# Performance work log

Hardware: AMD Instinct MI355X
Metric: run time of the kernel (lower is better)

## Reference

```python
import jax, jax.numpy as jnp
import numpy as np

N = 100000   # nodes
R = 4        # relation types
E = 200000   # edges per relation
IN, HID, OUT = 128, 256, 256


def _hetero_conv(x, ew, src, dst, W, b):
    """One HeteroGraphConv(mean) layer of GraphConv(norm='both') per relation.
    x: [N, d_in], ew: [R, E, d_in], src/dst: [R, E], W: [R, d_in, d_out], b: [R, d_out]."""
    outs = []
    for r in range(R):  # small fixed relation set
        s, d = src[r], dst[r]
        ones = jnp.ones((E,), x.dtype)
        deg_out = jax.ops.segment_sum(ones, s, num_segments=N)
        deg_in = jax.ops.segment_sum(ones, d, num_segments=N)
        ns = jax.lax.rsqrt(jnp.clip(deg_out, 1.0))  # src-side norm
        nd = jax.lax.rsqrt(jnp.clip(deg_in, 1.0))   # dst-side norm
        # gather src feats, scale, edge-weight, scatter-sum to dst
        m = x[s] * ns[s][:, None] * ew[r]                       # [E, d_in]
        agg = jax.ops.segment_sum(m, d, num_segments=N)          # [N, d_in]
        agg = agg * nd[:, None]
        outs.append(agg @ W[r] + b[r])
    return sum(outs) / R


def setup_inputs() -> dict:
    key = jax.random.key(0)
    ks = jax.random.split(key, 12)
    sc = 0.05
    return {
        "node_feat": jax.random.normal(ks[0], (N, IN), jnp.float32),
        "edge_w_raw": jax.random.normal(ks[1], (R, E, IN), jnp.float32),
        "src": jax.random.randint(ks[2], (R, E), 0, N),
        "dst": jax.random.randint(ks[3], (R, E), 0, N),
        "Wn": jax.random.normal(ks[4], (IN, HID), jnp.float32) * sc,
        "bn": jax.random.normal(ks[5], (HID,), jnp.float32) * sc,
        "Wr": jax.random.normal(ks[6], (IN, HID), jnp.float32) * sc,
        "br": jax.random.normal(ks[7], (HID,), jnp.float32) * sc,
        "W1": jax.random.normal(ks[8], (R, HID, HID), jnp.float32) * sc,
        "b1": jax.random.normal(ks[9], (R, HID), jnp.float32) * sc,
        "W2": jax.random.normal(ks[10], (R, HID, OUT), jnp.float32) * sc,
        "b2": jax.random.normal(ks[11], (R, OUT), jnp.float32) * sc,
    }


def reference(node_feat, edge_w_raw, src, dst, Wn, bn, Wr, br, W1, b1, W2, b2):
    # rela_fc on raw edge weights (shared by both layers)
    ew = jnp.einsum('rei,ih->reh', edge_w_raw, Wr) + br          # [R, E, HID]
    # node_fc
    x0 = node_feat @ Wn + bn                                      # [N, HID]
    h1 = _hetero_conv(x0, ew, src, dst, W1, b1)                   # [N, HID]
    h2 = _hetero_conv(h1, ew, src, dst, W2, b2)                   # [N, OUT]
    return h2
```

## Files before the change

### kernel.cpp

```cpp
#include <hip/hip_runtime.h>

constexpr int Nn  = 100000;
constexpr int Rr  = 4;
constexpr int Ee  = 200000;
constexpr int Din = 128;
constexpr int Dh  = 256;
constexpr int RN  = Rr * Nn;
constexpr int RE  = Rr * Ee;

typedef float  f32x4  __attribute__((ext_vector_type(4)));
typedef __bf16 bf16x4 __attribute__((ext_vector_type(4)));
typedef __bf16 bf16x8 __attribute__((ext_vector_type(8)));

__global__ __launch_bounds__(256) void count_deg_kernel(
    const int* __restrict__ src, const int* __restrict__ dst,
    int* __restrict__ dego, int* __restrict__ degi) {
  int i = blockIdx.x * 256 + threadIdx.x;
  if (i < RE) {
    int r = i / Ee;
    atomicAdd(&dego[r * Nn + src[i]], 1);
    atomicAdd(&degi[r * Nn + dst[i]], 1);
  }
}

__global__ __launch_bounds__(256) void norms_kernel(
    const int* __restrict__ dego, const int* __restrict__ degi,
    float* __restrict__ ns, float* __restrict__ nd) {
  int i = blockIdx.x * 256 + threadIdx.x;
  if (i < RN) {
    int a = dego[i]; if (a < 1) a = 1;
    int b = degi[i]; if (b < 1) b = 1;
    ns[i] = rsqrtf((float)a);
    nd[i] = rsqrtf((float)b);
  }
}

__device__ inline int block_excl_scan_256(int tsum, int tid, int* wsum) {
  int lane = tid & 63, w = tid >> 6;
  int inc = tsum;
#pragma unroll
  for (int off = 1; off < 64; off <<= 1) {
    int t = __shfl_up(inc, off);
    if (lane >= off) inc += t;
  }
  if (lane == 63) wsum[w] = inc;
  __syncthreads();
  int woff = 0;
  for (int i = 0; i < w; ++i) woff += wsum[i];
  return woff + inc - tsum;
}

__global__ __launch_bounds__(256) void scan1_kernel(
    const int* __restrict__ in, int* __restrict__ out,
    int* __restrict__ partials, int n) {
  __shared__ int wsum[4];
  int tid = threadIdx.x;
  int base = blockIdx.x * 1024 + tid * 4;
  int v[4];
#pragma unroll
  for (int j = 0; j < 4; ++j) v[j] = (base + j < n) ? in[base + j] : 0;
  int tsum = v[0] + v[1] + v[2] + v[3];
  int off = block_excl_scan_256(tsum, tid, wsum);
  int run = off;
#pragma unroll
  for (int j = 0; j < 4; ++j) {
    if (base + j < n) out[base + j] = run;
    run += v[j];
  }
  __syncthreads();
  if (tid == 0) partials[blockIdx.x] = wsum[0] + wsum[1] + wsum[2] + wsum[3];
}

__global__ __launch_bounds__(256) void scan2_kernel(int* __restrict__ p, int n) {
  __shared__ int wsum[4];
  int tid = threadIdx.x;
  int e0 = (2 * tid     < n) ? p[2 * tid]     : 0;
  int e1 = (2 * tid + 1 < n) ? p[2 * tid + 1] : 0;
  int off = block_excl_scan_256(e0 + e1, tid, wsum);
  if (2 * tid     < n) p[2 * tid]     = off;
  if (2 * tid + 1 < n) p[2 * tid + 1] = off + e0;
}

__global__ __launch_bounds__(256) void scan3_kernel(
    int* __restrict__ out, const int* __restrict__ partials, int n) {
  int i = blockIdx.x * 256 + threadIdx.x;
  if (i < n) out[i] += partials[i >> 10];
  if (i == 0) out[n] = RE;
}

__global__ __launch_bounds__(256) void fill_eid_kernel(
    const int* __restrict__ dst, int* __restrict__ cursor,
    int* __restrict__ eid) {
  int i = blockIdx.x * 256 + threadIdx.x;
  if (i < RE) {
    int r = i / Ee;
    int pos = atomicAdd(&cursor[r * Nn + dst[i]], 1);
    eid[pos] = i;
  }
}

__global__ __launch_bounds__(256) void bias_combine_kernel(
    const float* __restrict__ b1, const float* __restrict__ b2,
    float* __restrict__ cb) {
  int i = threadIdx.x;
  cb[i]      = 0.25f * (b1[i] + b1[Dh + i] + b1[2 * Dh + i] + b1[3 * Dh + i]);
  cb[Dh + i] = 0.25f * (b2[i] + b2[Dh + i] + b2[2 * Dh + i] + b2[3 * Dh + i]);
}

__global__ __launch_bounds__(256) void transpose_bf16_kernel(
    const float* __restrict__ in, __bf16* __restrict__ outp, int K) {
  __shared__ float t[32][33];
  int kb = blockIdx.x * 32, nb = blockIdx.y * 32;
  int tx = threadIdx.x & 31, ty = threadIdx.x >> 5;
#pragma unroll
  for (int j = 0; j < 32; j += 8)
    t[ty + j][tx] = in[(size_t)(kb + ty + j) * Dh + nb + tx];
  __syncthreads();
#pragma unroll
  for (int j = 0; j < 32; j += 8)
    outp[(size_t)(nb + ty + j) * K + kb + tx] = (__bf16)t[tx][ty + j];
}

template <int K, bool ABF16, bool OUT_BF16>
__global__ __launch_bounds__(256) void gemm_stream(
    const void* __restrict__ Av, const __bf16* __restrict__ Bt,
    void* __restrict__ Cv, const float* __restrict__ bias,
    float alpha, int M) {
  const int tid  = threadIdx.x;
  const int w    = tid >> 6;
  const int lane = tid & 63;
  const int l15  = lane & 15, quad = lane >> 4;
  const int m0   = blockIdx.x * 64;
  const int n0   = w * 64;

  f32x4 acc[4][4] = {};

  int arow[4];
#pragma unroll
  for (int mt = 0; mt < 4; ++mt) {
    int r = m0 + mt * 16 + l15;
    arow[mt] = (r < M) ? r : (M - 1);
  }

#pragma unroll 4
  for (int kt = 0; kt < K / 32; ++kt) {
    const int kk = kt * 32 + quad * 8;
    bf16x8 bfrag[4];
#pragma unroll
    for (int nt = 0; nt < 4; ++nt) {
      int n = n0 + nt * 16 + l15;
      bfrag[nt] = *(const bf16x8*)(Bt + (size_t)n * K + kk);
    }
    bf16x8 afrag[4];
    if constexpr (ABF16) {
      const __bf16* A = (const __bf16*)Av;
#pragma unroll
      for (int mt = 0; mt < 4; ++mt)
        afrag[mt] = *(const bf16x8*)(A + (size_t)arow[mt] * K + kk);
    } else {
      const float* A = (const float*)Av;
#pragma unroll
      for (int mt = 0; mt < 4; ++mt) {
        const float* ap = A + (size_t)arow[mt] * K + kk;
        f32x4 v0 = *(const f32x4*)(ap);
        f32x4 v1 = *(const f32x4*)(ap + 4);
        bf16x8 t;
        t[0] = (__bf16)v0[0]; t[1] = (__bf16)v0[1];
        t[2] = (__bf16)v0[2]; t[3] = (__bf16)v0[3];
        t[4] = (__bf16)v1[0]; t[5] = (__bf16)v1[1];
        t[6] = (__bf16)v1[2]; t[7] = (__bf16)v1[3];
        afrag[mt] = t;
      }
    }
#pragma unroll
    for (int mt = 0; mt < 4; ++mt)
#pragma unroll
      for (int nt = 0; nt < 4; ++nt)
        acc[mt][nt] = __builtin_amdgcn_mfma_f32_16x16x32_bf16(
            afrag[mt], bfrag[nt], acc[mt][nt], 0, 0, 0);
  }

#pragma unroll
  for (int mt = 0; mt < 4; ++mt) {
    int rl = m0 + mt * 16 + quad * 4;
#pragma unroll
    for (int nt = 0; nt < 4; ++nt) {
      int col = n0 + nt * 16 + l15;
      float bv = bias ? bias[col] : 0.f;
#pragma unroll
      for (int ri = 0; ri < 4; ++ri) {
        int grow = rl + ri;
        if (grow < M) {
          size_t idx = (size_t)grow * Dh + col;
          float v = alpha * acc[mt][nt][ri] + bv;
          if constexpr (OUT_BF16) {
            ((__bf16*)Cv)[idx] = (__bf16)v;
          } else {
            ((float*)Cv)[idx] = v;
          }
        }
      }
    }
  }
}

__global__ __launch_bounds__(256) void aggregate4_kernel(
    const float* __restrict__ x, const __bf16* __restrict__ ew,
    const int* __restrict__ src, const int* __restrict__ rowptr,
    const int* __restrict__ eid, const float* __restrict__ ns,
    const float* __restrict__ nd, __bf16* __restrict__ agg4) {
  int g = blockIdx.x * 4 + (threadIdx.x >> 6);
  if (g >= RN) return;
  int r = g / Nn;
  int n = g - r * Nn;
  int lane = threadIdx.x & 63;
  int p0 = rowptr[g], p1 = rowptr[g + 1];
  const float* nsr = ns + (size_t)r * Nn;
  f32x4 acc = {0.f, 0.f, 0.f, 0.f};
  for (int p = p0; p < p1; p += 2) {
    int  geA  = eid[p];
    bool hasB = (p + 1 < p1);
    int  geB  = hasB ? eid[p + 1] : geA;
    int sA = src[geA];
    int sB = src[geB];
    float scA = nsr[sA];
    float scB = hasB ? nsr[sB] : 0.f;
    f32x4  xA = *(const f32x4*)(x + (size_t)sA * Dh + lane * 4);
    bf16x4 eA = *(const bf16x4*)(ew + (size_t)geA * Dh + lane * 4);
    f32x4  xB = *(const f32x4*)(x + (size_t)sB * Dh + lane * 4);
    bf16x4 eB = *(const bf16x4*)(ew + (size_t)geB * Dh + lane * 4);
    acc[0] += xA[0] * scA * (float)eA[0] + xB[0] * scB * (float)eB[0];
    acc[1] += xA[1] * scA * (float)eA[1] + xB[1] * scB * (float)eB[1];
    acc[2] += xA[2] * scA * (float)eA[2] + xB[2] * scB * (float)eB[2];
    acc[3] += xA[3] * scA * (float)eA[3] + xB[3] * scB * (float)eB[3];
  }
  float ndv = nd[g];
  bf16x4 o;
  o[0] = (__bf16)(acc[0] * ndv);
  o[1] = (__bf16)(acc[1] * ndv);
  o[2] = (__bf16)(acc[2] * ndv);
  o[3] = (__bf16)(acc[3] * ndv);
  *(bf16x4*)(agg4 + (size_t)n * (4 * Dh) + (size_t)r * Dh + lane * 4) = o;
}

__global__ __launch_bounds__(256) void edge_scatter_kernel(
    const float* __restrict__ x, const __bf16* __restrict__ ew,
    const int* __restrict__ src, const int* __restrict__ dst,
    const float* __restrict__ ns, const float* __restrict__ nd,
    float* __restrict__ aggf, int cnt) {
  int e = blockIdx.x * 4 + (threadIdx.x >> 6);
  if (e >= cnt) return;
  int lane = threadIdx.x & 63;
  int s = src[e], d = dst[e];
  float sc = ns[s] * nd[d];
  f32x4 xv = *(const f32x4*)(x + (size_t)s * Dh + lane * 4);
  bf16x4 ev = *(const bf16x4*)(ew + (size_t)e * Dh + lane * 4);
  float* ap = aggf + (size_t)d * Dh + lane * 4;
  atomicAdd(ap + 0, xv[0] * sc * (float)ev[0]);
  atomicAdd(ap + 1, xv[1] * sc * (float)ev[1]);
  atomicAdd(ap + 2, xv[2] * sc * (float)ev[2]);
  atomicAdd(ap + 3, xv[3] * sc * (float)ev[3]);
}

__global__ __launch_bounds__(256) void pack_agg_kernel(
    const float* __restrict__ aggf, __bf16* __restrict__ agg4, int r) {
  int i = blockIdx.x * 256 + threadIdx.x;
  if (i < Nn * 64) {
    int n = i >> 6;
    int c = (i & 63) * 4;
    f32x4 v = *(const f32x4*)(aggf + (size_t)n * Dh + c);
    bf16x4 o;
    o[0] = (__bf16)v[0]; o[1] = (__bf16)v[1];
    o[2] = (__bf16)v[2]; o[3] = (__bf16)v[3];
    *(bf16x4*)(agg4 + (size_t)n * (4 * Dh) + (size_t)r * Dh + c) = o;
  }
}

extern "C" void kernel_launch(void* const* d_in, const int* in_sizes, int n_in,
                              void* d_out, int out_size, void* d_ws, size_t ws_size,
                              hipStream_t stream) {
  const float* node_feat  = (const float*)d_in[0];
  const float* edge_w_raw = (const float*)d_in[1];
  const int*   src        = (const int*)d_in[2];
  const int*   dst        = (const int*)d_in[3];
  const float* Wn = (const float*)d_in[4];
  const float* bn = (const float*)d_in[5];
  const float* Wr = (const float*)d_in[6];
  const float* br = (const float*)d_in[7];
  const float* W1 = (const float*)d_in[8];
  const float* b1 = (const float*)d_in[9];
  const float* W2 = (const float*)d_in[10];
  const float* b2 = (const float*)d_in[11];
  float* out = (float*)d_out;

  char* ws = (char*)d_ws;
  size_t off = 0;
  auto alloc = [&](size_t bytes) -> void* {
    void* p = ws + off;
    off += (bytes + 255) & ~(size_t)255;
    return p;
  };
  float*  ns     = (float*)alloc(sizeof(float) * RN);
  float*  nd     = (float*)alloc(sizeof(float) * RN);
  int*    rowptr = (int*)alloc(sizeof(int) * (RN + 1));
  int*    cursor = (int*)alloc(sizeof(int) * RN);
  int*    eid    = (int*)alloc(sizeof(int) * RE);
  int*    parts  = (int*)alloc(sizeof(int) * 512);
  float*  cb     = (float*)alloc(sizeof(float) * 2 * Dh);
  __bf16* BtWn   = (__bf16*)alloc(sizeof(__bf16) * (size_t)Din * Dh);
  __bf16* BtWr   = (__bf16*)alloc(sizeof(__bf16) * (size_t)Din * Dh);
  __bf16* BtW1   = (__bf16*)alloc(sizeof(__bf16) * (size_t)(4 * Dh) * Dh);
  __bf16* BtW2   = (__bf16*)alloc(sizeof(__bf16) * (size_t)(4 * Dh) * Dh);
  float*  x0     = (float*)alloc(sizeof(float) * (size_t)Nn * Dh);
  float*  h1     = (float*)alloc(sizeof(float) * (size_t)Nn * Dh);
  __bf16* agg4   = (__bf16*)alloc(sizeof(__bf16) * (size_t)Nn * 4 * Dh);
  size_t fixed = off;
  size_t ew_full_bytes = (size_t)RE * Dh * 2;
  bool full = (fixed + ew_full_bytes) <= ws_size;
  __bf16* ewb  = nullptr;
  float*  aggf = nullptr;
  int CH = Ee;
  if (full) {
    ewb = (__bf16*)alloc(ew_full_bytes);
  } else {
    aggf = (float*)alloc(sizeof(float) * (size_t)Nn * Dh);
    size_t avail = ws_size > off ? ws_size - off : 0;
    size_t ch = avail / ((size_t)Dh * 2);
    ch = (ch / 512) * 512;
    if (ch > (size_t)Ee) ch = (size_t)Ee;
    if (ch < 512) ch = 512;
    CH = (int)ch;
    ewb = (__bf16*)alloc((size_t)CH * Dh * 2);
  }

  int* dego = (int*)agg4;
  int* degi = dego + RN;
  hipMemsetAsync(dego, 0, sizeof(int) * 2 * (size_t)RN, stream);
  count_deg_kernel<<<(RE + 255) / 256, 256, 0, stream>>>(src, dst, dego, degi);
  norms_kernel<<<(RN + 255) / 256, 256, 0, stream>>>(dego, degi, ns, nd);

  int nchunks = (RN + 1023) / 1024;
  scan1_kernel<<<nchunks, 256, 0, stream>>>(degi, rowptr, parts, RN);
  scan2_kernel<<<1, 256, 0, stream>>>(parts, nchunks);
  scan3_kernel<<<(RN + 255) / 256, 256, 0, stream>>>(rowptr, parts, RN);
  hipMemcpyAsync(cursor, rowptr, sizeof(int) * RN, hipMemcpyDeviceToDevice, stream);
  fill_eid_kernel<<<(RE + 255) / 256, 256, 0, stream>>>(dst, cursor, eid);

  bias_combine_kernel<<<1, 256, 0, stream>>>(b1, b2, cb);
  transpose_bf16_kernel<<<dim3(Din / 32, Dh / 32), 256, 0, stream>>>(Wn, BtWn, Din);
  transpose_bf16_kernel<<<dim3(Din / 32, Dh / 32), 256, 0, stream>>>(Wr, BtWr, Din);
  transpose_bf16_kernel<<<dim3(4 * Dh / 32, Dh / 32), 256, 0, stream>>>(W1, BtW1, 4 * Dh);
  transpose_bf16_kernel<<<dim3(4 * Dh / 32, Dh / 32), 256, 0, stream>>>(W2, BtW2, 4 * Dh);

  gemm_stream<Din, false, false><<<(Nn + 63) / 64, 256, 0, stream>>>(
      node_feat, BtWn, x0, bn, 1.0f, Nn);

  if (full) {
    gemm_stream<Din, false, true><<<RE / 64, 256, 0, stream>>>(
        edge_w_raw, BtWr, ewb, br, 1.0f, RE);
  }

  for (int layer = 0; layer < 2; ++layer) {
    const float*  x   = layer ? h1 : x0;
    float*        o   = layer ? out : h1;
    const __bf16* Bt  = layer ? BtW2 : BtW1;
    const float*  cbl = cb + layer * Dh;
    if (full) {
      aggregate4_kernel<<<(RN + 3) / 4, 256, 0, stream>>>(
          x, ewb, src, rowptr, eid, ns, nd, agg4);
    } else {
      for (int r = 0; r < Rr; ++r) {
        hipMemsetAsync(aggf, 0, sizeof(float) * (size_t)Nn * Dh, stream);
        for (int c0 = 0; c0 < Ee; c0 += CH) {
          int cnt = (Ee - c0 < CH) ? (Ee - c0) : CH;
          gemm_stream<Din, false, true><<<(cnt + 63) / 64, 256, 0, stream>>>(
              edge_w_raw + ((size_t)r * Ee + c0) * Din, BtWr, ewb, br, 1.0f, cnt);
          edge_scatter_kernel<<<(cnt + 3) / 4, 256, 0, stream>>>(
              x, ewb, src + (size_t)r * Ee + c0, dst + (size_t)r * Ee + c0,
              ns + (size_t)r * Nn, nd + (size_t)r * Nn, aggf, cnt);
        }
        pack_agg_kernel<<<(Nn * 64 + 255) / 256, 256, 0, stream>>>(aggf, agg4, r);
      }
    }
    gemm_stream<4 * Dh, true, false><<<(Nn + 63) / 64, 256, 0, stream>>>(
        agg4, Bt, o, cbl, 0.25f, Nn);
  }
}
```

Before: 2.146 ms.

## Rewrite GEMMs with double-buffered LDS staging and persistent tiles

Replaces the direct-from-global GEMM with a kernel that stages A tiles into swizzled LDS using global_load_lds and double-buffers them, so loads for the next tile or K-slice overlap the MFMA work on the current one. The f32-input GEMMs become persistent: a 512-block grid loops over M tiles and keeps the B fragments in registers across tiles. The bf16 K=1024 GEMM pipelines over K chunks. The cost is more LDS per block (up to 64KB), hand-placed waitcnt and barriers, and a risk of lower occupancy.

```diff
diff --git a/kernel.cpp b/kernel.cpp
--- a/kernel.cpp
+++ b/kernel.cpp
@@ -121,86 +121,172 @@
     outp[(size_t)(nb + ty + j) * K + kb + tx] = (__bf16)t[tx][ty + j];
 }
 
+typedef __attribute__((address_space(1))) const void* gas_p;
+typedef __attribute__((address_space(3))) void* las_p;
+
+__device__ inline void gload_lds16(const void* g, void* l) {
+  __builtin_amdgcn_global_load_lds((gas_p)g, (las_p)l, 16, 0, 0);
+}
+
+__device__ inline void barrier_sync() {
+  asm volatile("" ::: "memory");
+  __builtin_amdgcn_s_barrier();
+  __builtin_amdgcn_sched_barrier(0);
+  asm volatile("" ::: "memory");
+}
+
 template <int K, bool ABF16, bool OUT_BF16>
-__global__ __launch_bounds__(256) void gemm_stream(
+__global__ __launch_bounds__(256, 2) void gemm_pipe(
     const void* __restrict__ Av, const __bf16* __restrict__ Bt,
     void* __restrict__ Cv, const float* __restrict__ bias,
-    float alpha, int M) {
+    float alpha, int M, int mtiles) {
+  constexpr int BUFB = ABF16 ? 16384 : 32768;
+  constexpr int ROWB = ABF16 ? 256 : 512;
+  constexpr int EB   = ABF16 ? 2 : 4;
+  constexpr int G    = BUFB / (256 * 16);
+  __shared__ __align__(16) char smem[2][BUFB];
   const int tid  = threadIdx.x;
   const int w    = tid >> 6;
   const int lane = tid & 63;
   const int l15  = lane & 15, quad = lane >> 4;
-  const int m0   = blockIdx.x * 64;
   const int n0   = w * 64;
-
-  f32x4 acc[4][4] = {};
-
-  int arow[4];
-#pragma unroll
-  for (int mt = 0; mt < 4; ++mt) {
-    int r = m0 + mt * 16 + l15;
-    arow[mt] = (r < M) ? r : (M - 1);
-  }
-
-#pragma unroll 4
-  for (int kt = 0; kt < K / 32; ++kt) {
-    const int kk = kt * 32 + quad * 8;
-    bf16x8 bfrag[4];
-#pragma unroll
-    for (int nt = 0; nt < 4; ++nt) {
-      int n = n0 + nt * 16 + l15;
-      bfrag[nt] = *(const bf16x8*)(Bt + (size_t)n * K + kk);
+  const int sw   = (l15 & 7) << 4;
+  const char* Ab = (const char*)Av;
+
+  auto stage = [&](int buf, int m0, int k0elt) {
+#pragma unroll
+    for (int j = 0; j < G; ++j) {
+      int lin   = (j * 256 + tid) * 16;
+      int row   = lin / ROWB;
+      int inrow = lin - row * ROWB;
+      int swz   = inrow ^ ((row & 7) << 4);
+      int grow  = m0 + row;
+      if (grow > M - 1) grow = M - 1;
+      gload_lds16(Ab + (size_t)grow * (K * EB) + (size_t)k0elt * EB + swz,
+                  &smem[buf][lin]);
     }
-    bf16x8 afrag[4];
-    if constexpr (ABF16) {
-      const __bf16* A = (const __bf16*)Av;
-#pragma unroll
-      for (int mt = 0; mt < 4; ++mt)
-        afrag[mt] = *(const bf16x8*)(A + (size_t)arow[mt] * K + kk);
-    } else {
-      const float* A = (const float*)Av;
-#pragma unroll
-      for (int mt = 0; mt < 4; ++mt) {
-        const float* ap = A + (size_t)arow[mt] * K + kk;
-        f32x4 v0 = *(const f32x4*)(ap);
-        f32x4 v1 = *(const f32x4*)(ap + 4);
-        bf16x8 t;
-        t[0] = (__bf16)v0[0]; t[1] = (__bf16)v0[1];
-        t[2] = (__bf16)v0[2]; t[3] = (__bf16)v0[3];
-        t[4] = (__bf16)v1[0]; t[5] = (__bf16)v1[1];
-        t[6] = (__bf16)v1[2]; t[7] = (__bf16)v1[3];
-        afrag[mt] = t;
-      }
-    }
-#pragma unroll
-    for (int mt = 0; mt < 4; ++mt)
-#pragma unroll
-      for (int nt = 0; nt < 4; ++nt)
-        acc[mt][nt] = __builtin_amdgcn_mfma_f32_16x16x32_bf16(
-            afrag[mt], bfrag[nt], acc[mt][nt], 0, 0, 0);
-  }
-
-#pragma unroll
-  for (int mt = 0; mt < 4; ++mt) {
-    int rl = m0 + mt * 16 + quad * 4;
-#pragma unroll
-    for (int nt = 0; nt < 4; ++nt) {
-      int col = n0 + nt * 16 + l15;
-      float bv = bias ? bias[col] : 0.f;
-#pragma unroll
-      for (int ri = 0; ri < 4; ++ri) {
-        int grow = rl + ri;
-        if (grow < M) {
-          size_t idx = (size_t)grow * Dh + col;
-          float v = alpha * acc[mt][nt][ri] + bv;
-          if constexpr (OUT_BF16) {
-            ((__bf16*)Cv)[idx] = (__bf16)v;
-          } else {
-            ((float*)Cv)[idx] = v;
+  };
+
+  auto store_tile = [&](f32x4 (&acc)[4][4], int m0) {
+#pragma unroll
+    for (int mtf = 0; mtf < 4; ++mtf) {
+      int rl = m0 + mtf * 16 + quad * 4;
+#pragma unroll
+      for (int nt = 0; nt < 4; ++nt) {
+        int col = n0 + nt * 16 + l15;
+        float bv = bias ? bias[col] : 0.f;
+#pragma unroll
+        for (int ri = 0; ri < 4; ++ri) {
+          int grow = rl + ri;
+          if (grow < M) {
+            size_t idx = (size_t)grow * Dh + col;
+            float v = alpha * acc[mtf][nt][ri] + bv;
+            if constexpr (OUT_BF16) ((__bf16*)Cv)[idx] = (__bf16)v;
+            else                    ((float*)Cv)[idx]  = v;
           }
         }
       }
     }
+  };
+
+  if constexpr (!ABF16) {
+    static_assert(K == 128, "f32 path expects K=128");
+    int t = blockIdx.x;
+    if (t >= mtiles) return;
+    stage(0, t * 64, 0);
+    bf16x8 bq[4][4];
+#pragma unroll
+    for (int ks = 0; ks < 4; ++ks)
+#pragma unroll
+      for (int nt = 0; nt < 4; ++nt)
+        bq[ks][nt] = *(const bf16x8*)(
+            Bt + (size_t)(n0 + nt * 16 + l15) * K + ks * 32 + quad * 8);
+    int cur = 0;
+    while (true) {
+      int tn = t + gridDim.x;
+      bool more = tn < mtiles;
+      if (more) {
+        stage(cur ^ 1, tn * 64, 0);
+        asm volatile("s_waitcnt vmcnt(%0)" :: "n"(G) : "memory");
+      } else {
+        asm volatile("s_waitcnt vmcnt(0)" ::: "memory");
+      }
+      barrier_sync();
+      const char* buf = smem[cur];
+      f32x4 acc[4][4] = {};
+      bf16x8 a[4][4];
+#pragma unroll
+      for (int mtf = 0; mtf < 4; ++mtf)
+#pragma unroll
+        for (int ks = 0; ks < 4; ++ks) {
+          int y  = (mtf * 16 + l15) * 512 + ks * 128 + quad * 32;
+          int ph = y ^ sw;
+          f32x4 v0 = *(const f32x4*)(buf + ph);
+          f32x4 v1 = *(const f32x4*)(buf + (ph ^ 16));
+          bf16x8 tt;
+          tt[0] = (__bf16)v0[0]; tt[1] = (__bf16)v0[1];
+          tt[2] = (__bf16)v0[2]; tt[3] = (__bf16)v0[3];
+          tt[4] = (__bf16)v1[0]; tt[5] = (__bf16)v1[1];
+          tt[6] = (__bf16)v1[2]; tt[7] = (__bf16)v1[3];
+          a[mtf][ks] = tt;
+        }
+#pragma unroll
+      for (int mtf = 0; mtf < 4; ++mtf)
+#pragma unroll
+        for (int nt = 0; nt < 4; ++nt)
+#pragma unroll
+          for (int ks = 0; ks < 4; ++ks)
+            acc[mtf][nt] = __builtin_amdgcn_mfma_f32_16x16x32_bf16(
+                a[mtf][ks], bq[ks][nt], acc[mtf][nt], 0, 0, 0);
+      store_tile(acc, t * 64);
+      barrier_sync();
+      if (!more) break;
+      cur ^= 1; t = tn;
+    }
+  } else {
+    static_assert(K == 1024, "bf16 path expects K=1024");
+    int m0 = blockIdx.x * 64;
+    stage(0, m0, 0);
+    f32x4 acc[4][4] = {};
+    int cur = 0;
+#pragma unroll 1
+    for (int kt = 0; kt < K / 128; ++kt) {
+      bool more = kt < K / 128 - 1;
+      if (more) {
+        stage(cur ^ 1, m0, (kt + 1) * 128);
+        asm volatile("s_waitcnt vmcnt(%0)" :: "n"(G) : "memory");
+      } else {
+        asm volatile("s_waitcnt vmcnt(0)" ::: "memory");
+      }
+      barrier_sync();
+      const char* buf = smem[cur];
+      bf16x8 bq[4][4];
+#pragma unroll
+      for (int ks = 0; ks < 4; ++ks)
+#pragma unroll
+        for (int nt = 0; nt < 4; ++nt)
+          bq[ks][nt] = *(const bf16x8*)(
+              Bt + (size_t)(n0 + nt * 16 + l15) * K + kt * 128 + ks * 32 + quad * 8);
+      bf16x8 a[4][4];
+#pragma unroll
+      for (int mtf = 0; mtf < 4; ++mtf)
+#pragma unroll
+        for (int ks = 0; ks < 4; ++ks) {
+          int y = (mtf * 16 + l15) * 256 + ks * 64 + quad * 16;
+          a[mtf][ks] = *(const bf16x8*)(buf + (y ^ sw));
+        }
+#pragma unroll
+      for (int mtf = 0; mtf < 4; ++mtf)
+#pragma unroll
+        for (int nt = 0; nt < 4; ++nt)
+#pragma unroll
+          for (int ks = 0; ks < 4; ++ks)
+            acc[mtf][nt] = __builtin_amdgcn_mfma_f32_16x16x32_bf16(
+                a[mtf][ks], bq[ks][nt], acc[mtf][nt], 0, 0, 0);
+      barrier_sync();
+      cur ^= 1;
+    }
+    store_tile(acc, m0);
   }
 }
 
@@ -352,12 +438,17 @@
   transpose_bf16_kernel<<<dim3(4 * Dh / 32, Dh / 32), 256, 0, stream>>>(W1, BtW1, 4 * Dh);
   transpose_bf16_kernel<<<dim3(4 * Dh / 32, Dh / 32), 256, 0, stream>>>(W2, BtW2, 4 * Dh);
 
-  gemm_stream<Din, false, false><<<(Nn + 63) / 64, 256, 0, stream>>>(
-      node_feat, BtWn, x0, bn, 1.0f, Nn);
+  {
+    int mt = (Nn + 63) / 64;
+    int g = mt < 512 ? mt : 512;
+    gemm_pipe<Din, false, false><<<g, 256, 0, stream>>>(
+        node_feat, BtWn, x0, bn, 1.0f, Nn, mt);
+  }
 
   if (full) {
-    gemm_stream<Din, false, true><<<RE / 64, 256, 0, stream>>>(
-        edge_w_raw, BtWr, ewb, br, 1.0f, RE);
+    int mt = RE / 64;
+    gemm_pipe<Din, false, true><<<512, 256, 0, stream>>>(
+        edge_w_raw, BtWr, ewb, br, 1.0f, RE, mt);
   }
 
   for (int layer = 0; layer < 2; ++layer) {
@@ -373,8 +464,10 @@
         hipMemsetAsync(aggf, 0, sizeof(float) * (size_t)Nn * Dh, stream);
         for (int c0 = 0; c0 < Ee; c0 += CH) {
           int cnt = (Ee - c0 < CH) ? (Ee - c0) : CH;
-          gemm_stream<Din, false, true><<<(cnt + 63) / 64, 256, 0, stream>>>(
-              edge_w_raw + ((size_t)r * Ee + c0) * Din, BtWr, ewb, br, 1.0f, cnt);
+          int mt = (cnt + 63) / 64;
+          int g = mt < 512 ? mt : 512;
+          gemm_pipe<Din, false, true><<<g, 256, 0, stream>>>(
+              edge_w_raw + ((size_t)r * Ee + c0) * Din, BtWr, ewb, br, 1.0f, cnt, mt);
           edge_scatter_kernel<<<(cnt + 3) / 4, 256, 0, stream>>>(
               x, ewb, src + (size_t)r * Ee + c0, dst + (size_t)r * Ee + c0,
               ns + (size_t)r * Nn, nd + (size_t)r * Nn, aggf, cnt);
@@ -382,7 +475,7 @@
         pack_agg_kernel<<<(Nn * 64 + 255) / 256, 256, 0, stream>>>(aggf, agg4, r);
       }
     }
-    gemm_stream<4 * Dh, true, false><<<(Nn + 63) / 64, 256, 0, stream>>>(
-        agg4, Bt, o, cbl, 0.25f, Nn);
-  }
-}
+    gemm_pipe<4 * Dh, true, false><<<(Nn + 63) / 64, 256, 0, stream>>>(
+        agg4, Bt, o, cbl, 0.25f, Nn, (Nn + 63) / 64);
+  }
+}
```

After: 1.819 ms. 1.18x faster.
